# Performance work log

Measured on AMD Instinct MI355X. Metric: run time of the kernel, lower is better.

The kernel has to match this reference:

```python
import jax, jax.numpy as jnp
import numpy as np

T, B, IN, H1, H2, OUT = 1024, 512, 20, 128, 64, 3

def _uniform(key, shape, bound):
    return jax.random.uniform(key, shape, jnp.float32, -bound, bound)

def setup_inputs() -> dict:
    key = jax.random.key(0)
    ks = jax.random.split(key, 11)
    b1 = 1.0 / np.sqrt(H1)
    b2 = 1.0 / np.sqrt(H2)
    return {
        "x": jax.random.normal(ks[0], (T, B, IN), jnp.float32),
        "W_ih0": _uniform(ks[1], (4 * H1, IN), b1),
        "W_hh0": _uniform(ks[2], (4 * H1, H1), b1),
        "b_ih0": _uniform(ks[3], (4 * H1,), b1),
        "b_hh0": _uniform(ks[4], (4 * H1,), b1),
        "W_ih1": _uniform(ks[5], (4 * H2, H1), b2),
        "W_hh1": _uniform(ks[6], (4 * H2, H2), b2),
        "b_ih1": _uniform(ks[7], (4 * H2,), b2),
        "b_hh1": _uniform(ks[8], (4 * H2,), b2),
        "W_d": _uniform(ks[9], (OUT, H2), b2),
        "b_d": _uniform(ks[10], (OUT,), b2),
    }

def _lstm_layer(x, W_ih, W_hh, b_ih, b_hh, hidden):
    # x: (T, B, in_dim); PyTorch gate order: i, f, g, o
    batch = x.shape[1]
    x_proj = jnp.einsum("tbi,gi->tbg", x, W_ih) + (b_ih + b_hh)  # (T,B,4H)

    def step(carry, xp):
        h, c = carry
        gates = xp + h @ W_hh.T  # (B,4H)
        i, f, g, o = jnp.split(gates, 4, axis=-1)
        i = jax.nn.sigmoid(i)
        f = jax.nn.sigmoid(f)
        g = jnp.tanh(g)
        o = jax.nn.sigmoid(o)
        c = f * c + i * g
        h = o * jnp.tanh(c)
        return (h, c), h

    h0 = jnp.zeros((batch, hidden), x.dtype)
    c0 = jnp.zeros((batch, hidden), x.dtype)
    _, ys = jax.lax.scan(step, (h0, c0), x_proj)
    return ys  # (T, B, H)

def reference(x, W_ih0, W_hh0, b_ih0, b_hh0, W_ih1, W_hh1, b_ih1, b_hh1, W_d, b_d):
    h1 = _lstm_layer(x, W_ih0, W_hh0, b_ih0, b_hh0, H1)   # (T,B,128)
    h2 = _lstm_layer(h1, W_ih1, W_hh1, b_ih1, b_hh1, H2)  # (T,B,64)
    # Faithful to original: lstm_out[:, -1, :] in seq-first layout picks the
    # last batch element at every timestep -> (T, 64)
    last = h2[:, -1, :]
    act = jax.nn.relu(last)
    # Dropout in eval mode is identity.
    return act @ W_d.T + b_d  # (T, 3)
```

## Files before the change

kernel.cpp:

```cpp
#include <hip/hip_runtime.h>
#include <hip/hip_bf16.h>


#define T_STEPS 1024
#define BATCH   512
#define IN_F    20
#define H1_     128
#define H2_     64
#define OUT_F   3
#define G1_     (4*H1_)
#define G2_     (4*H2_)

typedef float f4 __attribute__((ext_vector_type(4)));
typedef unsigned int u32;
typedef u32 u4 __attribute__((ext_vector_type(4)));
typedef _Float16 h2t __attribute__((ext_vector_type(2)));

__device__ __forceinline__ float sigmoidf_(float x) {
    return 1.0f / (1.0f + __expf(-x));
}
__device__ __forceinline__ float tanhf_(float x) {
    return 1.0f - 2.0f / (__expf(2.0f * x) + 1.0f);
}
__device__ __forceinline__ h2t as_h2(u32 v) {
    union { u32 u; h2t h; } c; c.u = v; return c.h;
}
__device__ __forceinline__ u32 pkh(float a, float b) {
    union { _Float16 h[2]; u32 u; } c;
    c.h[0] = (_Float16)a; c.h[1] = (_Float16)b; return c.u;
}
__device__ __forceinline__ float fdot2_(h2t a, h2t b, float c) {
#if __has_builtin(__builtin_amdgcn_fdot2)
    return __builtin_amdgcn_fdot2(a, b, c, false);
#else
    float d = c;
    asm("v_dot2_f32_f16 %0, %1, %2, %0" : "+v"(d) : "v"(a), "v"(b));
    return d;
#endif
}
__device__ __forceinline__ u4 packq(const float* p) {
    const f4 a = *(const f4*)p;
    const f4 b = *(const f4*)(p + 4);
    u4 pk;
    pk.x = pkh(a.x, a.y); pk.y = pkh(a.z, a.w);
    pk.z = pkh(b.x, b.y); pk.w = pkh(b.z, b.w);
    return pk;
}

#define LO_SCALE_INV 0.000244140625f

#define DOTQ(WQ, HH, HL)                                                      \
    { const u4 hh_ = (HH); const u4 hl_ = (HL);                               \
      a0 = fdot2_(as_h2((WQ).x), as_h2(hh_.x), a0);                           \
      a1 = fdot2_(as_h2((WQ).y), as_h2(hh_.y), a1);                           \
      a0 = fdot2_(as_h2((WQ).z), as_h2(hh_.z), a0);                           \
      a1 = fdot2_(as_h2((WQ).w), as_h2(hh_.w), a1);                           \
      a2 = fdot2_(as_h2((WQ).x), as_h2(hl_.x), a2);                           \
      a3 = fdot2_(as_h2((WQ).y), as_h2(hl_.y), a3);                           \
      a2 = fdot2_(as_h2((WQ).z), as_h2(hl_.z), a2);                           \
      a3 = fdot2_(as_h2((WQ).w), as_h2(hl_.w), a3); }

__global__ void xproj_kernel(const float* __restrict__ x,
                             const float* __restrict__ W_ih0,
                             const float* __restrict__ b_ih0,
                             const float* __restrict__ b_hh0,
                             float* __restrict__ xp1)
{
    const int t = blockIdx.x;
    const int g = threadIdx.x;
    const float* xr = x + ((size_t)t * BATCH + (BATCH - 1)) * IN_F;
    const float* w  = W_ih0 + g * IN_F;
    float acc = b_ih0[g] + b_hh0[g];
#pragma unroll
    for (int i = 0; i < IN_F; ++i) acc = fmaf(xr[i], w[i], acc);
    xp1[t * G1_ + g] = acc;
}

__global__ void pack_kernel(const float* __restrict__ W_hh0,
                            const float* __restrict__ W_hh1,
                            u4* __restrict__ wpk1,
                            u4* __restrict__ wpk2)
{
    const int idx = blockIdx.x * blockDim.x + threadIdx.x;
    if (idx < 4096) {
        const int r = idx >> 2, qq = idx & 3;
        const int g = r & 511, hf = r >> 9;
        wpk1[r * 4 + qq] = packq(W_hh0 + (size_t)g * H1_ + hf * 64 + 32 + 8 * qq);
    } else if (idx < 4096 + 1024) {
        const int i2 = idx - 4096;
        const int r2 = i2 >> 1, qq = i2 & 1;
        const int g2 = r2 & 255, hf = r2 >> 8;
        wpk2[r2 * 2 + qq] = packq(W_hh1 + (size_t)g2 * H2_ + hf * 32 + 16 + 8 * qq);
    }
}

__global__ __attribute__((amdgpu_flat_work_group_size(1024, 1024),
                          amdgpu_waves_per_eu(4, 4)))
void lstm1_kernel(const float* __restrict__ xp1,
                  const float* __restrict__ W_hh0,
                  const u4* __restrict__ wpk1,
                  float* __restrict__ h1seq)
{
    const int tid = threadIdx.x;
    const int g   = tid & 511;
    const int hf  = tid >> 9;
    const int r   = hf * 512 + g;

    __shared__ u4    swW[1024 * 5];
    __shared__ u4    shhi[16];
    __shared__ u4    shlo[16];
    __shared__ float sp1[1024];

    {
        const float* wr = W_hh0 + (size_t)g * H1_ + hf * 64;
#pragma unroll
        for (int q = 0; q < 4; ++q) swW[r * 5 + q] = packq(wr + q * 8);
    }
    if (tid < 16) { shhi[tid] = u4{0,0,0,0}; shlo[tid] = u4{0,0,0,0}; }
    float c1 = 0.0f;
    __syncthreads();

    const u4* wk = wpk1 + (size_t)r * 4;
    float xp_cur = (hf == 0) ? xp1[g] : 0.0f;

    for (int t = 0; t < T_STEPS; ++t) {
        float xp_next = 0.0f;
        if (hf == 0) {
            const int tn = (t + 1 < T_STEPS) ? (t + 1) : (T_STEPS - 1);
            xp_next = xp1[(size_t)tn * G1_ + g];
        }
        const u4 w4_ = wk[0], w5_ = wk[1], w6_ = wk[2], w7_ = wk[3];

        float a0 = 0.f, a1 = 0.f, a2 = 0.f, a3 = 0.f;
#pragma unroll
        for (int q = 0; q < 4; ++q) {
            const u4 wq = swW[r * 5 + q];
            DOTQ(wq, shhi[hf * 8 + q], shlo[hf * 8 + q]);
        }
        DOTQ(w4_, shhi[hf * 8 + 4], shlo[hf * 8 + 4]);
        DOTQ(w5_, shhi[hf * 8 + 5], shlo[hf * 8 + 5]);
        DOTQ(w6_, shhi[hf * 8 + 6], shlo[hf * 8 + 6]);
        DOTQ(w7_, shhi[hf * 8 + 7], shlo[hf * 8 + 7]);

        sp1[g * 2 + hf] = ((a0 + a1) + LO_SCALE_INV * (a2 + a3)) + xp_cur;
        __syncthreads();

        if (tid < H1_) {
            const float vi = sp1[tid * 2]              + sp1[tid * 2 + 1];
            const float vf = sp1[(H1_ + tid) * 2]      + sp1[(H1_ + tid) * 2 + 1];
            const float vg = sp1[(2 * H1_ + tid) * 2]  + sp1[(2 * H1_ + tid) * 2 + 1];
            const float vo = sp1[(3 * H1_ + tid) * 2]  + sp1[(3 * H1_ + tid) * 2 + 1];
            c1 = fmaf(sigmoidf_(vf), c1, sigmoidf_(vi) * tanhf_(vg));
            const float h = sigmoidf_(vo) * tanhf_(c1);
            const _Float16 hh16 = (_Float16)h;
            const float hrem = (h - (float)hh16) * 4096.0f;
            ((_Float16*)shhi)[tid] = hh16;
            ((_Float16*)shlo)[tid] = (_Float16)hrem;
            h1seq[(size_t)t * H1_ + tid] = h;
        }
        __syncthreads();
        xp_cur = xp_next;
    }
}

__global__ void xproj2_kernel(const float* __restrict__ h1seq,
                              const float* __restrict__ W_ih1,
                              const float* __restrict__ b_ih1,
                              const float* __restrict__ b_hh1,
                              float* __restrict__ xp2)
{
    const int t = blockIdx.x;
    const int g = threadIdx.x;
    __shared__ f4 sh[H1_ / 4];
    if (g < H1_ / 4) sh[g] = ((const f4*)(h1seq + (size_t)t * H1_))[g];
    __syncthreads();
    const f4* w = (const f4*)(W_ih1 + (size_t)g * H1_);
    float ax = 0.f, ay = 0.f, az = 0.f, aw = 0.f;
#pragma unroll
    for (int k = 0; k < H1_ / 4; ++k) {
        const f4 h4 = sh[k]; const f4 w4 = w[k];
        ax = fmaf(w4.x, h4.x, ax); ay = fmaf(w4.y, h4.y, ay);
        az = fmaf(w4.z, h4.z, az); aw = fmaf(w4.w, h4.w, aw);
    }
    xp2[(size_t)t * G2_ + g] = ((ax + ay) + (az + aw)) + b_ih1[g] + b_hh1[g];
}

__global__ __attribute__((amdgpu_flat_work_group_size(512, 512),
                          amdgpu_waves_per_eu(2, 2)))
void lstm2_kernel(const float* __restrict__ xp2,
                  const float* __restrict__ W_hh1,
                  const u4* __restrict__ wpk2,
                  float* __restrict__ h2seq)
{
    const int tid = threadIdx.x;
    const int g2  = tid & 255;
    const int hf  = tid >> 8;
    const int r2  = hf * 256 + g2;

    __shared__ u4    swW2[512 * 3];
    __shared__ u4    shhi[8];
    __shared__ u4    shlo[8];
    __shared__ float sp2[512];

    {
        const float* wr = W_hh1 + (size_t)g2 * H2_ + hf * 32;
        swW2[r2 * 3 + 0] = packq(wr);
        swW2[r2 * 3 + 1] = packq(wr + 8);
    }
    if (tid < 8) { shhi[tid] = u4{0,0,0,0}; shlo[tid] = u4{0,0,0,0}; }
    float c2 = 0.0f;
    __syncthreads();

    const u4* wk = wpk2 + (size_t)r2 * 2;
    float xp_cur = (hf == 0) ? xp2[g2] : 0.0f;

    for (int t = 0; t < T_STEPS; ++t) {
        float xp_next = 0.0f;
        if (hf == 0) {
            const int tn = (t + 1 < T_STEPS) ? (t + 1) : (T_STEPS - 1);
            xp_next = xp2[(size_t)tn * G2_ + g2];
        }
        const u4 w2_ = wk[0], w3_ = wk[1];

        float a0 = 0.f, a1 = 0.f, a2 = 0.f, a3 = 0.f;
        {
            const u4 wq0 = swW2[r2 * 3 + 0];
            DOTQ(wq0, shhi[hf * 4 + 0], shlo[hf * 4 + 0]);
            const u4 wq1 = swW2[r2 * 3 + 1];
            DOTQ(wq1, shhi[hf * 4 + 1], shlo[hf * 4 + 1]);
        }
        DOTQ(w2_, shhi[hf * 4 + 2], shlo[hf * 4 + 2]);
        DOTQ(w3_, shhi[hf * 4 + 3], shlo[hf * 4 + 3]);

        sp2[g2 * 2 + hf] = ((a0 + a1) + LO_SCALE_INV * (a2 + a3)) + xp_cur;
        __syncthreads();

        if (tid < H2_) {
            const float vi = sp2[tid * 2]              + sp2[tid * 2 + 1];
            const float vf = sp2[(H2_ + tid) * 2]      + sp2[(H2_ + tid) * 2 + 1];
            const float vg = sp2[(2 * H2_ + tid) * 2]  + sp2[(2 * H2_ + tid) * 2 + 1];
            const float vo = sp2[(3 * H2_ + tid) * 2]  + sp2[(3 * H2_ + tid) * 2 + 1];
            c2 = fmaf(sigmoidf_(vf), c2, sigmoidf_(vi) * tanhf_(vg));
            const float h = sigmoidf_(vo) * tanhf_(c2);
            const _Float16 hh16 = (_Float16)h;
            const float hrem = (h - (float)hh16) * 4096.0f;
            ((_Float16*)shhi)[tid] = hh16;
            ((_Float16*)shlo)[tid] = (_Float16)hrem;
            h2seq[(size_t)t * H2_ + tid] = h;
        }
        __syncthreads();
        xp_cur = xp_next;
    }
}

__global__ void head_kernel(const float* __restrict__ h2seq,
                            const float* __restrict__ W_d,
                            const float* __restrict__ b_d,
                            float* __restrict__ out)
{
    const int idx = blockIdx.x * blockDim.x + threadIdx.x;
    if (idx >= T_STEPS * OUT_F) return;
    const int t = idx / OUT_F;
    const int o = idx - t * OUT_F;
    const float* hr = h2seq + (size_t)t * H2_;
    const float* w  = W_d + o * H2_;
    float acc = b_d[o];
#pragma unroll
    for (int j = 0; j < H2_; ++j) acc = fmaf(fmaxf(hr[j], 0.0f), w[j], acc);
    out[idx] = acc;
}

extern "C" void kernel_launch(void* const* d_in, const int* in_sizes, int n_in,
                              void* d_out, int out_size, void* d_ws, size_t ws_size,
                              hipStream_t stream) {
    const float* x     = (const float*)d_in[0];
    const float* W_ih0 = (const float*)d_in[1];
    const float* W_hh0 = (const float*)d_in[2];
    const float* b_ih0 = (const float*)d_in[3];
    const float* b_hh0 = (const float*)d_in[4];
    const float* W_ih1 = (const float*)d_in[5];
    const float* W_hh1 = (const float*)d_in[6];
    const float* b_ih1 = (const float*)d_in[7];
    const float* b_hh1 = (const float*)d_in[8];
    const float* W_d   = (const float*)d_in[9];
    const float* b_d   = (const float*)d_in[10];

    float* out   = (float*)d_out;
    float* xp1   = (float*)d_ws;
    float* h1seq = xp1 + (size_t)T_STEPS * G1_;
    float* h2seq = h1seq + (size_t)T_STEPS * H1_;
    u4*    wpk1  = (u4*)(h2seq + (size_t)T_STEPS * H2_);
    u4*    wpk2  = wpk1 + 1024 * 4;
    float* xp2   = xp1;

    hipLaunchKernelGGL(xproj_kernel, dim3(T_STEPS), dim3(G1_), 0, stream,
                       x, W_ih0, b_ih0, b_hh0, xp1);
    hipLaunchKernelGGL(pack_kernel, dim3(20), dim3(256), 0, stream,
                       W_hh0, W_hh1, wpk1, wpk2);
    hipLaunchKernelGGL(lstm1_kernel, dim3(1), dim3(1024), 0, stream,
                       xp1, W_hh0, wpk1, h1seq);
    hipLaunchKernelGGL(xproj2_kernel, dim3(T_STEPS), dim3(G2_), 0, stream,
                       h1seq, W_ih1, b_ih1, b_hh1, xp2);
    hipLaunchKernelGGL(lstm2_kernel, dim3(1), dim3(512), 0, stream,
                       xp2, W_hh1, wpk2, h2seq);
    hipLaunchKernelGGL(head_kernel, dim3((T_STEPS * OUT_F + 255) / 256), dim3(256),
                       0, stream, h2seq, W_d, b_d, out);
}
```

Baseline: 1.675 ms.

## Stream all recurrent weights from global with coalesced layout; widen LSTM2 to 1024 threads

Removes the LDS-resident half of the recurrent weights in both LSTM kernels. All packed fp16 W_hh chunks now come from a pre-packed global buffer, laid out so each chunk index is contiguous across threads for coalesced loads that should hit in L1/L2 every step. LSTM2 is also split four ways along K instead of two, using 1024 threads, and reduces partials with vector LDS reads. This cuts LDS traffic and bank pressure per step, at the cost of more global/cache loads per timestep on the serial critical path.

```diff
diff --git a/kernel.cpp b/kernel.cpp
--- a/kernel.cpp
+++ b/kernel.cpp
@@ -82,22 +82,21 @@
                             u4* __restrict__ wpk2)
 {
     const int idx = blockIdx.x * blockDim.x + threadIdx.x;
-    if (idx < 4096) {
-        const int r = idx >> 2, qq = idx & 3;
+    if (idx < 8192) {
+        const int q = idx >> 10, r = idx & 1023;
         const int g = r & 511, hf = r >> 9;
-        wpk1[r * 4 + qq] = packq(W_hh0 + (size_t)g * H1_ + hf * 64 + 32 + 8 * qq);
-    } else if (idx < 4096 + 1024) {
-        const int i2 = idx - 4096;
-        const int r2 = i2 >> 1, qq = i2 & 1;
-        const int g2 = r2 & 255, hf = r2 >> 8;
-        wpk2[r2 * 2 + qq] = packq(W_hh1 + (size_t)g2 * H2_ + hf * 32 + 16 + 8 * qq);
+        wpk1[idx] = packq(W_hh0 + (size_t)g * H1_ + hf * 64 + q * 8);
+    } else if (idx < 8192 + 2048) {
+        const int i2 = idx - 8192;
+        const int q = i2 >> 10, r2 = i2 & 1023;
+        const int g2 = r2 & 255, qf = r2 >> 8;
+        wpk2[i2] = packq(W_hh1 + (size_t)g2 * H2_ + qf * 16 + q * 8);
     }
 }
 
 __global__ __attribute__((amdgpu_flat_work_group_size(1024, 1024),
                           amdgpu_waves_per_eu(4, 4)))
 void lstm1_kernel(const float* __restrict__ xp1,
-                  const float* __restrict__ W_hh0,
                   const u4* __restrict__ wpk1,
                   float* __restrict__ h1seq)
 {
@@ -106,21 +105,15 @@
     const int hf  = tid >> 9;
     const int r   = hf * 512 + g;
 
-    __shared__ u4    swW[1024 * 5];
     __shared__ u4    shhi[16];
     __shared__ u4    shlo[16];
     __shared__ float sp1[1024];
 
-    {
-        const float* wr = W_hh0 + (size_t)g * H1_ + hf * 64;
-#pragma unroll
-        for (int q = 0; q < 4; ++q) swW[r * 5 + q] = packq(wr + q * 8);
-    }
     if (tid < 16) { shhi[tid] = u4{0,0,0,0}; shlo[tid] = u4{0,0,0,0}; }
     float c1 = 0.0f;
     __syncthreads();
 
-    const u4* wk = wpk1 + (size_t)r * 4;
+    const u4* wb = wpk1 + r;
     float xp_cur = (hf == 0) ? xp1[g] : 0.0f;
 
     for (int t = 0; t < T_STEPS; ++t) {
@@ -129,14 +122,16 @@
             const int tn = (t + 1 < T_STEPS) ? (t + 1) : (T_STEPS - 1);
             xp_next = xp1[(size_t)tn * G1_ + g];
         }
-        const u4 w4_ = wk[0], w5_ = wk[1], w6_ = wk[2], w7_ = wk[3];
+        const u4 w0_ = wb[0 * 1024], w1_ = wb[1 * 1024];
+        const u4 w2_ = wb[2 * 1024], w3_ = wb[3 * 1024];
+        const u4 w4_ = wb[4 * 1024], w5_ = wb[5 * 1024];
+        const u4 w6_ = wb[6 * 1024], w7_ = wb[7 * 1024];
 
         float a0 = 0.f, a1 = 0.f, a2 = 0.f, a3 = 0.f;
-#pragma unroll
-        for (int q = 0; q < 4; ++q) {
-            const u4 wq = swW[r * 5 + q];
-            DOTQ(wq, shhi[hf * 8 + q], shlo[hf * 8 + q]);
-        }
+        DOTQ(w0_, shhi[hf * 8 + 0], shlo[hf * 8 + 0]);
+        DOTQ(w1_, shhi[hf * 8 + 1], shlo[hf * 8 + 1]);
+        DOTQ(w2_, shhi[hf * 8 + 2], shlo[hf * 8 + 2]);
+        DOTQ(w3_, shhi[hf * 8 + 3], shlo[hf * 8 + 3]);
         DOTQ(w4_, shhi[hf * 8 + 4], shlo[hf * 8 + 4]);
         DOTQ(w5_, shhi[hf * 8 + 5], shlo[hf * 8 + 5]);
         DOTQ(w6_, shhi[hf * 8 + 6], shlo[hf * 8 + 6]);
@@ -185,61 +180,51 @@
     xp2[(size_t)t * G2_ + g] = ((ax + ay) + (az + aw)) + b_ih1[g] + b_hh1[g];
 }
 
-__global__ __attribute__((amdgpu_flat_work_group_size(512, 512),
-                          amdgpu_waves_per_eu(2, 2)))
+__global__ __attribute__((amdgpu_flat_work_group_size(1024, 1024),
+                          amdgpu_waves_per_eu(4, 4)))
 void lstm2_kernel(const float* __restrict__ xp2,
-                  const float* __restrict__ W_hh1,
                   const u4* __restrict__ wpk2,
                   float* __restrict__ h2seq)
 {
     const int tid = threadIdx.x;
     const int g2  = tid & 255;
-    const int hf  = tid >> 8;
-    const int r2  = hf * 256 + g2;
-
-    __shared__ u4    swW2[512 * 3];
+    const int qf  = tid >> 8;
+
     __shared__ u4    shhi[8];
     __shared__ u4    shlo[8];
-    __shared__ float sp2[512];
-
-    {
-        const float* wr = W_hh1 + (size_t)g2 * H2_ + hf * 32;
-        swW2[r2 * 3 + 0] = packq(wr);
-        swW2[r2 * 3 + 1] = packq(wr + 8);
-    }
+    __shared__ float sp2[1024];
+
     if (tid < 8) { shhi[tid] = u4{0,0,0,0}; shlo[tid] = u4{0,0,0,0}; }
     float c2 = 0.0f;
     __syncthreads();
 
-    const u4* wk = wpk2 + (size_t)r2 * 2;
-    float xp_cur = (hf == 0) ? xp2[g2] : 0.0f;
+    const u4* wb = wpk2 + tid;
+    float xp_cur = (qf == 0) ? xp2[g2] : 0.0f;
 
     for (int t = 0; t < T_STEPS; ++t) {
         float xp_next = 0.0f;
-        if (hf == 0) {
+        if (qf == 0) {
             const int tn = (t + 1 < T_STEPS) ? (t + 1) : (T_STEPS - 1);
             xp_next = xp2[(size_t)tn * G2_ + g2];
         }
-        const u4 w2_ = wk[0], w3_ = wk[1];
+        const u4 w0_ = wb[0], w1_ = wb[1024];
 
         float a0 = 0.f, a1 = 0.f, a2 = 0.f, a3 = 0.f;
-        {
-            const u4 wq0 = swW2[r2 * 3 + 0];
-            DOTQ(wq0, shhi[hf * 4 + 0], shlo[hf * 4 + 0]);
-            const u4 wq1 = swW2[r2 * 3 + 1];
-            DOTQ(wq1, shhi[hf * 4 + 1], shlo[hf * 4 + 1]);
-        }
-        DOTQ(w2_, shhi[hf * 4 + 2], shlo[hf * 4 + 2]);
-        DOTQ(w3_, shhi[hf * 4 + 3], shlo[hf * 4 + 3]);
-
-        sp2[g2 * 2 + hf] = ((a0 + a1) + LO_SCALE_INV * (a2 + a3)) + xp_cur;
+        DOTQ(w0_, shhi[qf * 2 + 0], shlo[qf * 2 + 0]);
+        DOTQ(w1_, shhi[qf * 2 + 1], shlo[qf * 2 + 1]);
+
+        sp2[g2 * 4 + qf] = ((a0 + a1) + LO_SCALE_INV * (a2 + a3)) + xp_cur;
         __syncthreads();
 
         if (tid < H2_) {
-            const float vi = sp2[tid * 2]              + sp2[tid * 2 + 1];
-            const float vf = sp2[(H2_ + tid) * 2]      + sp2[(H2_ + tid) * 2 + 1];
-            const float vg = sp2[(2 * H2_ + tid) * 2]  + sp2[(2 * H2_ + tid) * 2 + 1];
-            const float vo = sp2[(3 * H2_ + tid) * 2]  + sp2[(3 * H2_ + tid) * 2 + 1];
+            const f4 pi = ((const f4*)sp2)[tid];
+            const f4 pf = ((const f4*)sp2)[H2_ + tid];
+            const f4 pg = ((const f4*)sp2)[2 * H2_ + tid];
+            const f4 po = ((const f4*)sp2)[3 * H2_ + tid];
+            const float vi = (pi.x + pi.y) + (pi.z + pi.w);
+            const float vf = (pf.x + pf.y) + (pf.z + pf.w);
+            const float vg = (pg.x + pg.y) + (pg.z + pg.w);
+            const float vo = (po.x + po.y) + (po.z + po.w);
             c2 = fmaf(sigmoidf_(vf), c2, sigmoidf_(vi) * tanhf_(vg));
             const float h = sigmoidf_(vo) * tanhf_(c2);
             const _Float16 hh16 = (_Float16)h;
@@ -290,19 +275,19 @@
     float* h1seq = xp1 + (size_t)T_STEPS * G1_;
     float* h2seq = h1seq + (size_t)T_STEPS * H1_;
     u4*    wpk1  = (u4*)(h2seq + (size_t)T_STEPS * H2_);
-    u4*    wpk2  = wpk1 + 1024 * 4;
+    u4*    wpk2  = wpk1 + 8192;
     float* xp2   = xp1;
 
     hipLaunchKernelGGL(xproj_kernel, dim3(T_STEPS), dim3(G1_), 0, stream,
                        x, W_ih0, b_ih0, b_hh0, xp1);
-    hipLaunchKernelGGL(pack_kernel, dim3(20), dim3(256), 0, stream,
+    hipLaunchKernelGGL(pack_kernel, dim3(40), dim3(256), 0, stream,
                        W_hh0, W_hh1, wpk1, wpk2);
     hipLaunchKernelGGL(lstm1_kernel, dim3(1), dim3(1024), 0, stream,
-                       xp1, W_hh0, wpk1, h1seq);
+                       xp1, wpk1, h1seq);
     hipLaunchKernelGGL(xproj2_kernel, dim3(T_STEPS), dim3(G2_), 0, stream,
                        h1seq, W_ih1, b_ih1, b_hh1, xp2);
-    hipLaunchKernelGGL(lstm2_kernel, dim3(1), dim3(512), 0, stream,
-                       xp2, W_hh1, wpk2, h2seq);
+    hipLaunchKernelGGL(lstm2_kernel, dim3(1), dim3(1024), 0, stream,
+                       xp2, wpk2, h2seq);
     hipLaunchKernelGGL(head_kernel, dim3((T_STEPS * OUT_F + 255) / 256), dim3(256),
                        0, stream, h2seq, W_d, b_d, out);
 }
```

Result: faster. 1.625 ms (-3.0%).
